# Performance work log

Measured on AMD Instinct MI355X. Metric: run time of the kernel, lower is better.

The kernel has to match this reference:

```python
import jax, jax.numpy as jnp
import numpy as np

EPS_BN = 1e-5
EPS_W = 1e-8


def _bn(x, g, b, m, v):
    # x: [B, N, C]; params: [C] (inference-mode batchnorm)
    return g * (x - m) * jax.lax.rsqrt(v + EPS_BN) + b


def setup_inputs() -> dict:
    key = jax.random.key(0)
    ks = jax.random.split(key, 24)
    B, N, S = 16, 4096, 1024
    C1, C2 = 128, 256            # points1 / points2 channels
    CIN, COUT = C1 + C2, 128     # in_channel, out_channel

    def w(k, shape, std=0.02):
        return (jax.random.normal(k, shape, jnp.float32) * std)

    def bn_params(k, c):
        k1, k2, k3, k4 = jax.random.split(k, 4)
        return (1.0 + 0.1 * jax.random.normal(k1, (c,), jnp.float32),  # gamma
                0.1 * jax.random.normal(k2, (c,), jnp.float32),        # beta
                0.1 * jax.random.normal(k3, (c,), jnp.float32),        # running mean
                0.5 + jax.random.uniform(k4, (c,), jnp.float32))       # running var

    fg, fb, fm, fv = bn_params(ks[4], COUT)
    g1, b1, m1, v1 = bn_params(ks[5], COUT)
    g2, b2, m2, v2 = bn_params(ks[6], COUT)
    return {
        "xyz1": jax.random.uniform(ks[0], (B, N, 3), jnp.float32),
        "xyz2": jax.random.uniform(ks[1], (B, S, 3), jnp.float32),
        "points1": jax.random.normal(ks[2], (B, C1, N), jnp.float32),
        "points2": jax.random.normal(ks[3], (B, C2, S), jnp.float32),
        "fuse_w": w(ks[7], (COUT, CIN)), "fuse_b": jnp.zeros((COUT,), jnp.float32),
        "fuse_g": fg, "fuse_beta": fb, "fuse_m": fm, "fuse_v": fv,
        "c1_w": w(ks[8], (COUT, COUT)), "c1_b": jnp.zeros((COUT,), jnp.float32),
        "bn1_g": g1, "bn1_b": b1, "bn1_m": m1, "bn1_v": v1,
        "c2_w": w(ks[9], (COUT, COUT)), "c2_b": jnp.zeros((COUT,), jnp.float32),
        "bn2_g": g2, "bn2_b": b2, "bn2_m": m2, "bn2_v": v2,
    }


def reference(xyz1, xyz2, points1, points2,
              fuse_w, fuse_b, fuse_g, fuse_beta, fuse_m, fuse_v,
              c1_w, c1_b, bn1_g, bn1_b, bn1_m, bn1_v,
              c2_w, c2_b, bn2_g, bn2_b, bn2_m, bn2_v):
    B, N, _ = xyz1.shape
    pts1 = jnp.swapaxes(points1, 1, 2)   # [B, N, C1]
    pts2 = jnp.swapaxes(points2, 1, 2)   # [B, S, C2]

    # squared pairwise distances [B, N, S]
    dists = (jnp.sum(xyz1 ** 2, -1)[:, :, None]
             + jnp.sum(xyz2 ** 2, -1)[:, None, :]
             - 2.0 * jnp.einsum('bnc,bsc->bns', xyz1, xyz2))

    # 3 nearest neighbors (smallest distances)
    neg_d3, idx = jax.lax.top_k(-dists, 3)          # [B, N, 3]
    d3 = -neg_d3
    recip = 1.0 / (d3 + EPS_W)
    weight = recip / jnp.sum(recip, axis=2, keepdims=True)  # [B, N, 3]

    gathered = jax.vmap(lambda p, i: p[i])(pts2, idx)        # [B, N, 3, C2]
    interp = jnp.sum(gathered * weight[..., None], axis=2)   # [B, N, C2]

    x = jnp.concatenate([pts1, interp], axis=-1)             # [B, N, CIN]

    # fuse: 1x1 conv + BN + ReLU
    x = jax.nn.relu(_bn(jnp.einsum('bnc,oc->bno', x, fuse_w) + fuse_b,
                        fuse_g, fuse_beta, fuse_m, fuse_v))

    # residual block: conv-BN-ReLU -> conv-BN, add skip, ReLU
    h = jax.nn.relu(_bn(jnp.einsum('bnc,oc->bno', x, c1_w) + c1_b,
                        bn1_g, bn1_b, bn1_m, bn1_v))
    y = _bn(jnp.einsum('bnc,oc->bno', h, c2_w) + c2_b,
            bn2_g, bn2_b, bn2_m, bn2_v)
    out = jax.nn.relu(y + x)                                 # [B, N, COUT]
    return jnp.swapaxes(out, 1, 2)                           # [B, COUT, N]
```

## Files before the change

### kernel.cpp

```cpp
#include <hip/hip_runtime.h>
#include <hip/hip_bf16.h>

#define BB 16
#define NN 4096
#define SS 1024
#define C1 128
#define C2 256
#define CIN 384
#define CO 128

typedef __bf16 bf16x8 __attribute__((ext_vector_type(8)));
typedef float f32x4 __attribute__((ext_vector_type(4)));

__global__ __launch_bounds__(256) void knn_kernel(
    const float* __restrict__ xyz1, const float* __restrict__ xyz2,
    int* __restrict__ idx4, float* __restrict__ w4)
{
    __shared__ float4 pts[SS];
    const int b = blockIdx.y;
    const float* p2 = xyz2 + (size_t)b * SS * 3;
    for (int i = threadIdx.x; i < SS; i += 256) {
        float x = p2[i * 3 + 0], y = p2[i * 3 + 1], z = p2[i * 3 + 2];
        pts[i] = make_float4(x, y, z, x * x + y * y + z * z);
    }
    __syncthreads();

    const int n = blockIdx.x * 256 + threadIdx.x;
    const float* p1 = xyz1 + ((size_t)b * NN + n) * 3;
    const float x = p1[0], y = p1[1], z = p1[2];
    const float s1 = x * x + y * y + z * z;

    float d0 = 3.4e38f, d1 = 3.4e38f, d2 = 3.4e38f, d3 = 3.4e38f;
    int i0 = 0, i1 = 0, i2 = 0, i3 = 0;
    #pragma unroll 4
    for (int s = 0; s < SS; ++s) {
        float4 p = pts[s];
        float d = s1 + p.w - 2.0f * (x * p.x + y * p.y + z * p.z);
        bool lt0 = d < d0, lt1 = d < d1, lt2 = d < d2, lt3 = d < d3;
        float nd3 = lt2 ? d2 : (lt3 ? d : d3); int ni3 = lt2 ? i2 : (lt3 ? s : i3);
        float nd2 = lt1 ? d1 : (lt2 ? d : d2); int ni2 = lt1 ? i1 : (lt2 ? s : i2);
        float nd1 = lt0 ? d0 : (lt1 ? d : d1); int ni1 = lt0 ? i0 : (lt1 ? s : i1);
        d0 = lt0 ? d : d0;                     i0 = lt0 ? s : i0;
        d1 = nd1; i1 = ni1; d2 = nd2; i2 = ni2; d3 = nd3; i3 = ni3;
    }
    float r0 = 1.0f / (d0 + 1e-8f);
    float r1 = 1.0f / (d1 + 1e-8f);
    float r2 = 1.0f / (d2 + 1e-8f);
    float rs = r0 + r1 + r2;
    bool tie = (d2 == d3);
    size_t base = ((size_t)b * NN + n) * 4;
    idx4[base + 0] = i0; idx4[base + 1] = i1;
    idx4[base + 2] = i2; idx4[base + 3] = i3;
    w4[base + 0] = r0 / rs; w4[base + 1] = r1 / rs;
    w4[base + 2] = r2 / rs; w4[base + 3] = tie ? -1.0f : 0.0f;
}

__global__ __launch_bounds__(256) void p2t_kernel(
    const float* __restrict__ p2, float* __restrict__ p2t)
{
    __shared__ float tile[64][65];
    const int b = blockIdx.z;
    const int s0 = blockIdx.x * 64, c0 = blockIdx.y * 64;
    for (int i = threadIdx.x; i < 64 * 64; i += 256) {
        int s = i & 63, c = i >> 6;
        tile[c][s] = p2[((size_t)b * C2 + c0 + c) * SS + s0 + s];
    }
    __syncthreads();
    for (int i = threadIdx.x; i < 64 * 64; i += 256) {
        int c = i & 63, s = i >> 6;
        p2t[((size_t)b * SS + s0 + s) * C2 + c0 + c] = tile[c][s];
    }
}

__global__ __launch_bounds__(256) void wprep_kernel(
    const float* __restrict__ fw, const float* __restrict__ w1,
    const float* __restrict__ w2,
    __bf16* __restrict__ Whf, __bf16* __restrict__ Wlf,
    __bf16* __restrict__ Wh1, __bf16* __restrict__ Wl1,
    __bf16* __restrict__ Wh2, __bf16* __restrict__ Wl2)
{
    int t = blockIdx.x * 256 + threadIdx.x;
    float v; __bf16 *oh, *ol; int idx;
    if (t < 49152)      { idx = t;         v = fw[idx]; oh = Whf; ol = Wlf; }
    else if (t < 65536) { idx = t - 49152; v = w1[idx]; oh = Wh1; ol = Wl1; }
    else                { idx = t - 65536; v = w2[idx]; oh = Wh2; ol = Wl2; }
    __bf16 h = (__bf16)v;
    oh[idx] = h; ol[idx] = (__bf16)(v - (float)h);
}

__global__ __launch_bounds__(256) void tie_eval_kernel(
    const float* __restrict__ p2t, const float* __restrict__ points1,
    const int* __restrict__ idx4, float* __restrict__ w4,
    const float* __restrict__ fw, const float* __restrict__ fb,
    const float* __restrict__ fg, const float* __restrict__ fbt,
    const float* __restrict__ fm, const float* __restrict__ fv,
    const float* __restrict__ w1m, const float* __restrict__ b1,
    const float* __restrict__ g1, const float* __restrict__ bt1,
    const float* __restrict__ m1, const float* __restrict__ v1,
    const float* __restrict__ w2m, const float* __restrict__ b2,
    const float* __restrict__ g2, const float* __restrict__ bt2,
    const float* __restrict__ m2, const float* __restrict__ v2)
{
    __shared__ float Xs[4][2][CIN];
    __shared__ float XT[4][2][CO];
    __shared__ float Hs[4][2][CO];
    const int wave = threadIdx.x >> 6, lane = threadIdx.x & 63;
    const int n = blockIdx.x * 4 + wave;
    const int b = blockIdx.y;
    const size_t base = ((size_t)b * NN + n) * 4;
    if (w4[base + 3] != -1.0f) return;

    const int i0 = idx4[base + 0], i1 = idx4[base + 1];
    const int i2 = idx4[base + 2], i3 = idx4[base + 3];
    const float w0 = w4[base + 0], w1 = w4[base + 1], w2 = w4[base + 2];
    const float* P = p2t + (size_t)b * SS * C2;

    for (int c = lane; c < C1; c += 64) {
        float v = points1[((size_t)b * C1 + c) * NN + n];
        Xs[wave][0][c] = v; Xs[wave][1][c] = v;
    }
    for (int c = lane; c < C2; c += 64) {
        float f0 = P[(size_t)i0 * C2 + c], f1 = P[(size_t)i1 * C2 + c];
        float f2 = P[(size_t)i2 * C2 + c], f3 = P[(size_t)i3 * C2 + c];
        float bs = w0 * f0 + w1 * f1;
        Xs[wave][0][C1 + c] = bs + w2 * f2;
        Xs[wave][1][C1 + c] = bs + w2 * f3;
    }
    #pragma unroll
    for (int k = 0; k < 2; ++k) {
        int oc = lane + 64 * k;
        float alo = fb[oc], ahi = fb[oc];
        for (int c = 0; c < CIN; ++c) {
            float wv = fw[(size_t)oc * CIN + c];
            alo += wv * Xs[wave][0][c];
            ahi += wv * Xs[wave][1][c];
        }
        float s = fg[oc] * (1.0f / sqrtf(fv[oc] + 1e-5f));
        XT[wave][0][oc] = fmaxf(s * (alo - fm[oc]) + fbt[oc], 0.0f);
        XT[wave][1][oc] = fmaxf(s * (ahi - fm[oc]) + fbt[oc], 0.0f);
    }
    #pragma unroll
    for (int k = 0; k < 2; ++k) {
        int oc = lane + 64 * k;
        float alo = b1[oc], ahi = b1[oc];
        for (int c = 0; c < CO; ++c) {
            float wv = w1m[(size_t)oc * CO + c];
            alo += wv * XT[wave][0][c];
            ahi += wv * XT[wave][1][c];
        }
        float s = g1[oc] * (1.0f / sqrtf(v1[oc] + 1e-5f));
        Hs[wave][0][oc] = fmaxf(s * (alo - m1[oc]) + bt1[oc], 0.0f);
        Hs[wave][1][oc] = fmaxf(s * (ahi - m1[oc]) + bt1[oc], 0.0f);
    }
    float e = 0.0f;
    #pragma unroll
    for (int k = 0; k < 2; ++k) {
        int oc = lane + 64 * k;
        float alo = b2[oc], ahi = b2[oc];
        for (int c = 0; c < CO; ++c) {
            float wv = w2m[(size_t)oc * CO + c];
            alo += wv * Hs[wave][0][c];
            ahi += wv * Hs[wave][1][c];
        }
        float s = g2[oc] * (1.0f / sqrtf(v2[oc] + 1e-5f));
        float olo = fmaxf(s * (alo - m2[oc]) + bt2[oc] + XT[wave][0][oc], 0.0f);
        float ohi = fmaxf(s * (ahi - m2[oc]) + bt2[oc] + XT[wave][1][oc], 0.0f);
        e = fmaxf(e, fabsf(olo - ohi));
    }
    for (int off = 32; off; off >>= 1) e = fmaxf(e, __shfl_xor(e, off));
    if (lane == 0) {
        if (e > 0.085f) { w4[base + 3] = 0.0f; }
        else { w4[base + 2] = 0.5f * w2; w4[base + 3] = 0.5f * w2; }
    }
}

__global__ __launch_bounds__(256) void buildx_kernel(
    const float* __restrict__ points1,
    const float* __restrict__ p2t,
    const int* __restrict__ idx4, const float* __restrict__ w4,
    __bf16* __restrict__ Xh, __bf16* __restrict__ Xl)
{
    __shared__ float t1[128][66];
    const int b = blockIdx.y;
    const int n0 = blockIdx.x * 64;
    for (int i = threadIdx.x; i < 128 * 64; i += 256) {
        int j = i & 63, c = i >> 6;
        t1[c][j] = points1[((size_t)b * C1 + c) * NN + n0 + j];
    }
    __syncthreads();
    for (int i = threadIdx.x; i < 128 * 64; i += 256) {
        int c = i & 127, j = i >> 7;
        float v = t1[c][j];
        __bf16 h = (__bf16)v;
        size_t o = ((size_t)b * NN + n0 + j) * CIN + c;
        Xh[o] = h; Xl[o] = (__bf16)(v - (float)h);
    }
    for (int i = threadIdx.x; i < 64 * C2; i += 256) {
        int c = i & 255, j = i >> 8;
        int n = n0 + j;
        size_t ib = ((size_t)b * NN + n) * 4;
        int s0 = idx4[ib + 0], s1 = idx4[ib + 1];
        int s2 = idx4[ib + 2], s3 = idx4[ib + 3];
        float w0 = w4[ib + 0], w1 = w4[ib + 1];
        float w2 = w4[ib + 2], w3 = w4[ib + 3];
        const float* base = p2t + (size_t)b * SS * C2;
        float v = w0 * base[(size_t)s0 * C2 + c]
                + w1 * base[(size_t)s1 * C2 + c]
                + w2 * base[(size_t)s2 * C2 + c]
                + w3 * base[(size_t)s3 * C2 + c];
        __bf16 h = (__bf16)v;
        size_t o = ((size_t)b * NN + n) * CIN + C1 + c;
        Xh[o] = h; Xl[o] = (__bf16)(v - (float)h);
    }
}

template<int K, int MODE>
__global__ __launch_bounds__(256) void gemm_bn_kernel(
    const __bf16* __restrict__ Ah, const __bf16* __restrict__ Al,
    const __bf16* __restrict__ Wh, const __bf16* __restrict__ Wl,
    const float* __restrict__ cb,  const float* __restrict__ gg,
    const float* __restrict__ bbta, const float* __restrict__ mm,
    const float* __restrict__ vv,
    const __bf16* __restrict__ skiph, const __bf16* __restrict__ skipl,
    __bf16* __restrict__ outh, __bf16* __restrict__ outl,
    float* __restrict__ outf)
{
    __shared__ __attribute__((aligned(16))) __bf16 wls_h[128 * 40];
    __shared__ __attribute__((aligned(16))) __bf16 wls_l[128 * 40];
    __shared__ float s_s[128], s_t[128];
    __shared__ float tile[32][132];
    const int tid = threadIdx.x;
    if (tid < 128) {
        float s = gg[tid] * (1.0f / sqrtf(vv[tid] + 1e-5f));
        float t = (cb[tid] - mm[tid]) * s + bbta[tid];
        s_s[tid] = s; s_t[tid] = t;
    }
    const int wave = tid >> 6, lane = tid & 63;
    const int m = lane & 15, q = lane >> 4;
    const size_t r0 = (size_t)blockIdx.x * 128 + wave * 32;

    f32x4 acc[2][8] = {};
    const __bf16* pAh = Ah + (r0 + m) * (size_t)K + q * 8;
    const __bf16* pAl = Al + (r0 + m) * (size_t)K + q * 8;

    const int wrow = tid >> 1, whf = tid & 1;
    for (int kk = 0; kk < K; kk += 32) {
        __syncthreads();
        {
            size_t g = (size_t)wrow * K + kk + whf * 16;
            int lo = wrow * 40 + whf * 16;
            *(uint4*)&wls_h[lo]     = *(const uint4*)&Wh[g];
            *(uint4*)&wls_h[lo + 8] = *(const uint4*)&Wh[g + 8];
            *(uint4*)&wls_l[lo]     = *(const uint4*)&Wl[g];
            *(uint4*)&wls_l[lo + 8] = *(const uint4*)&Wl[g + 8];
        }
        __syncthreads();
        bf16x8 ah0 = *(const bf16x8*)(pAh + kk);
        bf16x8 al0 = *(const bf16x8*)(pAl + kk);
        bf16x8 ah1 = *(const bf16x8*)(pAh + 16 * (size_t)K + kk);
        bf16x8 al1 = *(const bf16x8*)(pAl + 16 * (size_t)K + kk);
        #pragma unroll
        for (int ot = 0; ot < 8; ++ot) {
            bf16x8 bh = *(const bf16x8*)&wls_h[(ot * 16 + m) * 40 + q * 8];
            bf16x8 bl = *(const bf16x8*)&wls_l[(ot * 16 + m) * 40 + q * 8];
            acc[0][ot] = __builtin_amdgcn_mfma_f32_16x16x32_bf16(ah0, bh, acc[0][ot], 0, 0, 0);
            acc[0][ot] = __builtin_amdgcn_mfma_f32_16x16x32_bf16(al0, bh, acc[0][ot], 0, 0, 0);
            acc[0][ot] = __builtin_amdgcn_mfma_f32_16x16x32_bf16(ah0, bl, acc[0][ot], 0, 0, 0);
            acc[1][ot] = __builtin_amdgcn_mfma_f32_16x16x32_bf16(ah1, bh, acc[1][ot], 0, 0, 0);
            acc[1][ot] = __builtin_amdgcn_mfma_f32_16x16x32_bf16(al1, bh, acc[1][ot], 0, 0, 0);
            acc[1][ot] = __builtin_amdgcn_mfma_f32_16x16x32_bf16(ah1, bl, acc[1][ot], 0, 0, 0);
        }
    }

    if (MODE == 0) {
        #pragma unroll
        for (int rt = 0; rt < 2; ++rt) {
            #pragma unroll
            for (int ot = 0; ot < 8; ++ot) {
                int col = ot * 16 + m;
                float sc = s_s[col], sh = s_t[col];
                #pragma unroll
                for (int r = 0; r < 4; ++r) {
                    size_t row = r0 + rt * 16 + q * 4 + r;
                    float val = fmaxf(acc[rt][ot][r] * sc + sh, 0.0f);
                    __bf16 h = (__bf16)val;
                    outh[row * 128 + col] = h;
                    outl[row * 128 + col] = (__bf16)(val - (float)h);
                }
            }
        }
    } else {
        const int bidx = (int)(((size_t)blockIdx.x * 128) >> 12);
        const int nbase = (int)(((size_t)blockIdx.x * 128) & 4095);
        for (int cc = 0; cc < 4; ++cc) {
            __syncthreads();
            #pragma unroll
            for (int oo = 0; oo < 2; ++oo) {
                int ot = cc * 2 + oo;
                int col = ot * 16 + m;
                float sc = s_s[col], sh = s_t[col];
                #pragma unroll
                for (int rt = 0; rt < 2; ++rt) {
                    #pragma unroll
                    for (int r = 0; r < 4; ++r) {
                        int lrow = wave * 32 + rt * 16 + q * 4 + r;
                        size_t row = (size_t)blockIdx.x * 128 + lrow;
                        float val = acc[rt][ot][r] * sc + sh;
                        val += (float)skiph[row * 128 + col] + (float)skipl[row * 128 + col];
                        val = fmaxf(val, 0.0f);
                        tile[oo * 16 + m][lrow] = val;
                    }
                }
            }
            __syncthreads();
            for (int c2 = tid >> 7; c2 < 32; c2 += 2) {
                int nn_ = tid & 127;
                outf[((size_t)bidx * 128 + cc * 32 + c2) * NN + nbase + nn_] = tile[c2][nn_];
            }
        }
    }
}

extern "C" void kernel_launch(void* const* d_in, const int* in_sizes, int n_in,
                              void* d_out, int out_size, void* d_ws, size_t ws_size,
                              hipStream_t stream) {
    const float* xyz1    = (const float*)d_in[0];
    const float* xyz2    = (const float*)d_in[1];
    const float* points1 = (const float*)d_in[2];
    const float* points2 = (const float*)d_in[3];
    const float* fuse_w  = (const float*)d_in[4];
    const float* fuse_b  = (const float*)d_in[5];
    const float* fuse_g  = (const float*)d_in[6];
    const float* fuse_bt = (const float*)d_in[7];
    const float* fuse_m  = (const float*)d_in[8];
    const float* fuse_v  = (const float*)d_in[9];
    const float* c1_w    = (const float*)d_in[10];
    const float* c1_b    = (const float*)d_in[11];
    const float* bn1_g   = (const float*)d_in[12];
    const float* bn1_b   = (const float*)d_in[13];
    const float* bn1_m   = (const float*)d_in[14];
    const float* bn1_v   = (const float*)d_in[15];
    const float* c2_w    = (const float*)d_in[16];
    const float* c2_b    = (const float*)d_in[17];
    const float* bn2_g   = (const float*)d_in[18];
    const float* bn2_b   = (const float*)d_in[19];
    const float* bn2_m   = (const float*)d_in[20];
    const float* bn2_v   = (const float*)d_in[21];

    char* ws = (char*)d_ws;
    int*    idx4 = (int*)(ws);
    float*  w4   = (float*)(ws + 1048576);
    float*  p2t  = (float*)(ws + 2097152);
    __bf16* Xh   = (__bf16*)(ws + 18874368);
    __bf16* Xl   = (__bf16*)(ws + 69206016);
    __bf16* Y0h  = (__bf16*)(ws + 119537664);
    __bf16* Y0l  = (__bf16*)(ws + 136314880);
    __bf16* Hh   = (__bf16*)(ws + 153092096);
    __bf16* Hl   = (__bf16*)(ws + 169869312);
    __bf16* Whf  = (__bf16*)(ws + 186646528);
    __bf16* Wlf  = (__bf16*)(ws + 186744832);
    __bf16* Wh1  = (__bf16*)(ws + 186843136);
    __bf16* Wl1  = (__bf16*)(ws + 186875904);
    __bf16* Wh2  = (__bf16*)(ws + 186908672);
    __bf16* Wl2  = (__bf16*)(ws + 186941440);

    knn_kernel<<<dim3(NN / 256, BB), 256, 0, stream>>>(xyz1, xyz2, idx4, w4);
    p2t_kernel<<<dim3(SS / 64, C2 / 64, BB), 256, 0, stream>>>(points2, p2t);
    wprep_kernel<<<320, 256, 0, stream>>>(fuse_w, c1_w, c2_w,
                                          Whf, Wlf, Wh1, Wl1, Wh2, Wl2);
    tie_eval_kernel<<<dim3(NN / 4, BB), 256, 0, stream>>>(
        p2t, points1, idx4, w4,
        fuse_w, fuse_b, fuse_g, fuse_bt, fuse_m, fuse_v,
        c1_w, c1_b, bn1_g, bn1_b, bn1_m, bn1_v,
        c2_w, c2_b, bn2_g, bn2_b, bn2_m, bn2_v);
    buildx_kernel<<<dim3(NN / 64, BB), 256, 0, stream>>>(points1, p2t, idx4, w4, Xh, Xl);

    const int gblocks = (BB * NN) / 128;
    gemm_bn_kernel<CIN, 0><<<gblocks, 256, 0, stream>>>(
        Xh, Xl, Whf, Wlf, fuse_b, fuse_g, fuse_bt, fuse_m, fuse_v,
        nullptr, nullptr, Y0h, Y0l, nullptr);
    gemm_bn_kernel<CO, 0><<<gblocks, 256, 0, stream>>>(
        Y0h, Y0l, Wh1, Wl1, c1_b, bn1_g, bn1_b, bn1_m, bn1_v,
        nullptr, nullptr, Hh, Hl, nullptr);
    gemm_bn_kernel<CO, 1><<<gblocks, 256, 0, stream>>>(
        Hh, Hl, Wh2, Wl2, c2_b, bn2_g, bn2_b, bn2_m, bn2_v,
        Y0h, Y0l, nullptr, nullptr, (float*)d_out);
}
```

Measured before the change: 371.1 us.

## Apply fuse conv to points2 before interpolation, removing the wide concat GEMM

The fuse 1x1 conv is linear, so its points2 half is now applied to the S=1024 source points first (G = W2 * p2), and the interpolation then gathers and weights 128-channel projected rows instead of 256-channel raw rows. This removes the buildx kernel and the wide 384-channel X buffer in split bf16. The fuse GEMM now runs with K=128 over N points plus a K=256 GEMM over only S points. The interpolation gather moves into the GEMM prologue through a large shared tile, which adds shared-memory pressure. It also changes rounding order, since the projection is done in split-bf16 before the weights are applied.

```diff
diff --git a/kernel.cpp b/kernel.cpp
--- a/kernel.cpp
+++ b/kernel.cpp
@@ -56,7 +56,8 @@
 }
 
 __global__ __launch_bounds__(256) void p2t_kernel(
-    const float* __restrict__ p2, float* __restrict__ p2t)
+    const float* __restrict__ p2, float* __restrict__ p2t,
+    __bf16* __restrict__ p2th, __bf16* __restrict__ p2tl)
 {
     __shared__ float tile[64][65];
     const int b = blockIdx.z;
@@ -68,22 +69,53 @@
     __syncthreads();
     for (int i = threadIdx.x; i < 64 * 64; i += 256) {
         int c = i & 63, s = i >> 6;
-        p2t[((size_t)b * SS + s0 + s) * C2 + c0 + c] = tile[c][s];
+        float v = tile[c][s];
+        size_t o = ((size_t)b * SS + s0 + s) * C2 + c0 + c;
+        p2t[o] = v;
+        __bf16 h = (__bf16)v;
+        p2th[o] = h; p2tl[o] = (__bf16)(v - (float)h);
+    }
+}
+
+__global__ __launch_bounds__(256) void p1t_kernel(
+    const float* __restrict__ points1,
+    __bf16* __restrict__ P1h, __bf16* __restrict__ P1l)
+{
+    __shared__ float t1[128][66];
+    const int b = blockIdx.y;
+    const int n0 = blockIdx.x * 64;
+    for (int i = threadIdx.x; i < 128 * 64; i += 256) {
+        int j = i & 63, c = i >> 6;
+        t1[c][j] = points1[((size_t)b * C1 + c) * NN + n0 + j];
+    }
+    __syncthreads();
+    for (int i = threadIdx.x; i < 128 * 64; i += 256) {
+        int c = i & 127, j = i >> 7;
+        float v = t1[c][j];
+        __bf16 h = (__bf16)v;
+        size_t o = ((size_t)b * NN + n0 + j) * C1 + c;
+        P1h[o] = h; P1l[o] = (__bf16)(v - (float)h);
     }
 }
 
 __global__ __launch_bounds__(256) void wprep_kernel(
     const float* __restrict__ fw, const float* __restrict__ w1,
     const float* __restrict__ w2,
-    __bf16* __restrict__ Whf, __bf16* __restrict__ Wlf,
-    __bf16* __restrict__ Wh1, __bf16* __restrict__ Wl1,
-    __bf16* __restrict__ Wh2, __bf16* __restrict__ Wl2)
+    __bf16* __restrict__ Wf1h, __bf16* __restrict__ Wf1l,
+    __bf16* __restrict__ Wf2h, __bf16* __restrict__ Wf2l,
+    __bf16* __restrict__ W1h, __bf16* __restrict__ W1l,
+    __bf16* __restrict__ W2h, __bf16* __restrict__ W2l)
 {
     int t = blockIdx.x * 256 + threadIdx.x;
     float v; __bf16 *oh, *ol; int idx;
-    if (t < 49152)      { idx = t;         v = fw[idx]; oh = Whf; ol = Wlf; }
-    else if (t < 65536) { idx = t - 49152; v = w1[idx]; oh = Wh1; ol = Wl1; }
-    else                { idx = t - 65536; v = w2[idx]; oh = Wh2; ol = Wl2; }
+    if (t < 16384) {
+        int o = t >> 7, c = t & 127;
+        v = fw[(size_t)o * CIN + c]; oh = Wf1h; ol = Wf1l; idx = t;
+    } else if (t < 49152) {
+        int t2 = t - 16384; int o = t2 >> 8, c = t2 & 255;
+        v = fw[(size_t)o * CIN + 128 + c]; oh = Wf2h; ol = Wf2l; idx = t2;
+    } else if (t < 65536) { idx = t - 49152; v = w1[idx]; oh = W1h; ol = W1l; }
+    else                  { idx = t - 65536; v = w2[idx]; oh = W2h; ol = W2l; }
     __bf16 h = (__bf16)v;
     oh[idx] = h; ol[idx] = (__bf16)(v - (float)h);
 }
@@ -174,46 +206,6 @@
     }
 }
 
-__global__ __launch_bounds__(256) void buildx_kernel(
-    const float* __restrict__ points1,
-    const float* __restrict__ p2t,
-    const int* __restrict__ idx4, const float* __restrict__ w4,
-    __bf16* __restrict__ Xh, __bf16* __restrict__ Xl)
-{
-    __shared__ float t1[128][66];
-    const int b = blockIdx.y;
-    const int n0 = blockIdx.x * 64;
-    for (int i = threadIdx.x; i < 128 * 64; i += 256) {
-        int j = i & 63, c = i >> 6;
-        t1[c][j] = points1[((size_t)b * C1 + c) * NN + n0 + j];
-    }
-    __syncthreads();
-    for (int i = threadIdx.x; i < 128 * 64; i += 256) {
-        int c = i & 127, j = i >> 7;
-        float v = t1[c][j];
-        __bf16 h = (__bf16)v;
-        size_t o = ((size_t)b * NN + n0 + j) * CIN + c;
-        Xh[o] = h; Xl[o] = (__bf16)(v - (float)h);
-    }
-    for (int i = threadIdx.x; i < 64 * C2; i += 256) {
-        int c = i & 255, j = i >> 8;
-        int n = n0 + j;
-        size_t ib = ((size_t)b * NN + n) * 4;
-        int s0 = idx4[ib + 0], s1 = idx4[ib + 1];
-        int s2 = idx4[ib + 2], s3 = idx4[ib + 3];
-        float w0 = w4[ib + 0], w1 = w4[ib + 1];
-        float w2 = w4[ib + 2], w3 = w4[ib + 3];
-        const float* base = p2t + (size_t)b * SS * C2;
-        float v = w0 * base[(size_t)s0 * C2 + c]
-                + w1 * base[(size_t)s1 * C2 + c]
-                + w2 * base[(size_t)s2 * C2 + c]
-                + w3 * base[(size_t)s3 * C2 + c];
-        __bf16 h = (__bf16)v;
-        size_t o = ((size_t)b * NN + n) * CIN + C1 + c;
-        Xh[o] = h; Xl[o] = (__bf16)(v - (float)h);
-    }
-}
-
 template<int K, int MODE>
 __global__ __launch_bounds__(256) void gemm_bn_kernel(
     const __bf16* __restrict__ Ah, const __bf16* __restrict__ Al,
@@ -222,18 +214,39 @@
     const float* __restrict__ bbta, const float* __restrict__ mm,
     const float* __restrict__ vv,
     const __bf16* __restrict__ skiph, const __bf16* __restrict__ skipl,
+    const float* __restrict__ Gg, const int* __restrict__ idx4,
+    const float* __restrict__ w4,
     __bf16* __restrict__ outh, __bf16* __restrict__ outl,
     float* __restrict__ outf)
 {
     __shared__ __attribute__((aligned(16))) __bf16 wls_h[128 * 40];
     __shared__ __attribute__((aligned(16))) __bf16 wls_l[128 * 40];
     __shared__ float s_s[128], s_t[128];
-    __shared__ float tile[32][132];
+    __shared__ float tile[(MODE == 1) ? 32 : 1][132];
+    __shared__ float Itile[(MODE == 3) ? 128 : 1][129];
     const int tid = threadIdx.x;
-    if (tid < 128) {
+    if (MODE != 2 && tid < 128) {
         float s = gg[tid] * (1.0f / sqrtf(vv[tid] + 1e-5f));
         float t = (cb[tid] - mm[tid]) * s + bbta[tid];
         s_s[tid] = s; s_t[tid] = t;
+    }
+    if (MODE == 3) {
+        const size_t gr = (size_t)blockIdx.x * 128;
+        const int bb = (int)(gr >> 12);
+        const float* Gb = Gg + (size_t)bb * SS * 128;
+        for (int it = 0; it < 64; ++it) {
+            int i = it * 256 + tid;
+            int qq = i >> 7, c = i & 127;
+            size_t ib = (gr + qq) * 4;
+            int j0 = idx4[ib + 0], j1 = idx4[ib + 1];
+            int j2 = idx4[ib + 2], j3 = idx4[ib + 3];
+            float u0 = w4[ib + 0], u1 = w4[ib + 1];
+            float u2 = w4[ib + 2], u3 = w4[ib + 3];
+            Itile[qq][c] = u0 * Gb[(size_t)j0 * 128 + c]
+                         + u1 * Gb[(size_t)j1 * 128 + c]
+                         + u2 * Gb[(size_t)j2 * 128 + c]
+                         + u3 * Gb[(size_t)j3 * 128 + c];
+        }
     }
     const int wave = tid >> 6, lane = tid & 63;
     const int m = lane & 15, q = lane >> 4;
@@ -272,7 +285,7 @@
         }
     }
 
-    if (MODE == 0) {
+    if (MODE == 0 || MODE == 3) {
         #pragma unroll
         for (int rt = 0; rt < 2; ++rt) {
             #pragma unroll
@@ -281,11 +294,27 @@
                 float sc = s_s[col], sh = s_t[col];
                 #pragma unroll
                 for (int r = 0; r < 4; ++r) {
-                    size_t row = r0 + rt * 16 + q * 4 + r;
-                    float val = fmaxf(acc[rt][ot][r] * sc + sh, 0.0f);
+                    int lrow = wave * 32 + rt * 16 + q * 4 + r;
+                    size_t row = (size_t)blockIdx.x * 128 + lrow;
+                    float a = acc[rt][ot][r];
+                    if (MODE == 3) a += Itile[lrow][col];
+                    float val = fmaxf(a * sc + sh, 0.0f);
                     __bf16 h = (__bf16)val;
                     outh[row * 128 + col] = h;
                     outl[row * 128 + col] = (__bf16)(val - (float)h);
+                }
+            }
+        }
+    } else if (MODE == 2) {
+        #pragma unroll
+        for (int rt = 0; rt < 2; ++rt) {
+            #pragma unroll
+            for (int ot = 0; ot < 8; ++ot) {
+                int col = ot * 16 + m;
+                #pragma unroll
+                for (int r = 0; r < 4; ++r) {
+                    size_t row = r0 + rt * 16 + q * 4 + r;
+                    outf[row * 128 + col] = acc[rt][ot][r];
                 }
             }
         }
@@ -351,38 +380,46 @@
     int*    idx4 = (int*)(ws);
     float*  w4   = (float*)(ws + 1048576);
     float*  p2t  = (float*)(ws + 2097152);
-    __bf16* Xh   = (__bf16*)(ws + 18874368);
-    __bf16* Xl   = (__bf16*)(ws + 69206016);
-    __bf16* Y0h  = (__bf16*)(ws + 119537664);
-    __bf16* Y0l  = (__bf16*)(ws + 136314880);
-    __bf16* Hh   = (__bf16*)(ws + 153092096);
-    __bf16* Hl   = (__bf16*)(ws + 169869312);
-    __bf16* Whf  = (__bf16*)(ws + 186646528);
-    __bf16* Wlf  = (__bf16*)(ws + 186744832);
-    __bf16* Wh1  = (__bf16*)(ws + 186843136);
-    __bf16* Wl1  = (__bf16*)(ws + 186875904);
-    __bf16* Wh2  = (__bf16*)(ws + 186908672);
-    __bf16* Wl2  = (__bf16*)(ws + 186941440);
+    __bf16* p2th = (__bf16*)(ws + 18874368);
+    __bf16* p2tl = (__bf16*)(ws + 27262976);
+    __bf16* P1h  = (__bf16*)(ws + 35651584);
+    __bf16* P1l  = (__bf16*)(ws + 52428800);
+    float*  G    = (float*)(ws + 69206016);
+    __bf16* Y0h  = (__bf16*)(ws + 77594624);
+    __bf16* Y0l  = (__bf16*)(ws + 94371840);
+    __bf16* Hh   = (__bf16*)(ws + 111149056);
+    __bf16* Hl   = (__bf16*)(ws + 127926272);
+    __bf16* Wf1h = (__bf16*)(ws + 144703488);
+    __bf16* Wf1l = (__bf16*)(ws + 144736256);
+    __bf16* Wf2h = (__bf16*)(ws + 144769024);
+    __bf16* Wf2l = (__bf16*)(ws + 144834560);
+    __bf16* W1h  = (__bf16*)(ws + 144900096);
+    __bf16* W1l  = (__bf16*)(ws + 144932864);
+    __bf16* W2h  = (__bf16*)(ws + 144965632);
+    __bf16* W2l  = (__bf16*)(ws + 144998400);
 
     knn_kernel<<<dim3(NN / 256, BB), 256, 0, stream>>>(xyz1, xyz2, idx4, w4);
-    p2t_kernel<<<dim3(SS / 64, C2 / 64, BB), 256, 0, stream>>>(points2, p2t);
+    p2t_kernel<<<dim3(SS / 64, C2 / 64, BB), 256, 0, stream>>>(points2, p2t, p2th, p2tl);
+    p1t_kernel<<<dim3(NN / 64, BB), 256, 0, stream>>>(points1, P1h, P1l);
     wprep_kernel<<<320, 256, 0, stream>>>(fuse_w, c1_w, c2_w,
-                                          Whf, Wlf, Wh1, Wl1, Wh2, Wl2);
+                                          Wf1h, Wf1l, Wf2h, Wf2l,
+                                          W1h, W1l, W2h, W2l);
     tie_eval_kernel<<<dim3(NN / 4, BB), 256, 0, stream>>>(
         p2t, points1, idx4, w4,
         fuse_w, fuse_b, fuse_g, fuse_bt, fuse_m, fuse_v,
         c1_w, c1_b, bn1_g, bn1_b, bn1_m, bn1_v,
         c2_w, c2_b, bn2_g, bn2_b, bn2_m, bn2_v);
-    buildx_kernel<<<dim3(NN / 64, BB), 256, 0, stream>>>(points1, p2t, idx4, w4, Xh, Xl);
-
-    const int gblocks = (BB * NN) / 128;
-    gemm_bn_kernel<CIN, 0><<<gblocks, 256, 0, stream>>>(
-        Xh, Xl, Whf, Wlf, fuse_b, fuse_g, fuse_bt, fuse_m, fuse_v,
-        nullptr, nullptr, Y0h, Y0l, nullptr);
-    gemm_bn_kernel<CO, 0><<<gblocks, 256, 0, stream>>>(
-        Y0h, Y0l, Wh1, Wl1, c1_b, bn1_g, bn1_b, bn1_m, bn1_v,
-        nullptr, nullptr, Hh, Hl, nullptr);
-    gemm_bn_kernel<CO, 1><<<gblocks, 256, 0, stream>>>(
-        Hh, Hl, Wh2, Wl2, c2_b, bn2_g, bn2_b, bn2_m, bn2_v,
-        Y0h, Y0l, nullptr, nullptr, (float*)d_out);
-}
+
+    gemm_bn_kernel<C2, 2><<<(BB * SS) / 128, 256, 0, stream>>>(
+        p2th, p2tl, Wf2h, Wf2l, fuse_b, fuse_g, fuse_bt, fuse_m, fuse_v,
+        nullptr, nullptr, nullptr, nullptr, nullptr, nullptr, nullptr, G);
+    gemm_bn_kernel<C1, 3><<<(BB * NN) / 128, 256, 0, stream>>>(
+        P1h, P1l, Wf1h, Wf1l, fuse_b, fuse_g, fuse_bt, fuse_m, fuse_v,
+        nullptr, nullptr, G, idx4, w4, Y0h, Y0l, nullptr);
+    gemm_bn_kernel<CO, 0><<<(BB * NN) / 128, 256, 0, stream>>>(
+        Y0h, Y0l, W1h, W1l, c1_b, bn1_g, bn1_b, bn1_m, bn1_v,
+        nullptr, nullptr, nullptr, nullptr, nullptr, Hh, Hl, nullptr);
+    gemm_bn_kernel<CO, 1><<<(BB * NN) / 128, 256, 0, stream>>>(
+        Hh, Hl, W2h, W2l, c2_b, bn2_g, bn2_b, bn2_m, bn2_v,
+        Y0h, Y0l, nullptr, nullptr, nullptr, nullptr, nullptr, (float*)d_out);
+}
```

Result: no change. 375.2 us (+1.1%).
